# Performance work log

Measured on AMD Instinct MI355X. Metric: run time of the kernel, lower is better.

The kernel has to match this reference:

```python
import jax, jax.numpy as jnp
import numpy as np

B, Q, H = 1, 2048, 2048
NH, NKV, HD = 16, 8, 128
PAST = 2048
EPS = 1e-6


def rotate_half(x):
    x1, x2 = x[..., : x.shape[-1] // 2], x[..., x.shape[-1] // 2 :]
    return jnp.concatenate((-x2, x1), axis=-1)


def rms_norm(x, w, eps=EPS):
    var = jnp.mean(jnp.square(x.astype(jnp.float32)), axis=-1, keepdims=True)
    return (x * jax.lax.rsqrt(var + eps)) * w


def setup_inputs() -> dict:
    key = jax.random.key(0)
    ks = jax.random.split(key, 8)
    hidden_states = jax.random.normal(ks[0], (B, Q, H), jnp.float32)
    # RoPE tables for positions [PAST, PAST+Q)
    inv_freq = 1.0 / (1000000.0 ** (np.arange(0, HD, 2, dtype=np.float32) / HD))
    pos = np.arange(PAST, PAST + Q, dtype=np.float32)
    freqs = np.outer(pos, inv_freq)  # [Q, HD/2]
    emb = np.concatenate([freqs, freqs], axis=-1)  # [Q, HD]
    cos = jnp.asarray(np.cos(emb))[None].repeat(B, 0)
    sin = jnp.asarray(np.sin(emb))[None].repeat(B, 0)
    # causal additive mask over kv_len = PAST + Q
    q_idx = np.arange(Q)[:, None] + PAST
    kv_idx = np.arange(PAST + Q)[None, :]
    mask = np.where(kv_idx <= q_idx, 0.0, -1e9).astype(np.float32)
    attention_mask = jnp.asarray(mask)[None, None]  # [1,1,Q,PAST+Q]
    s = 1.0 / np.sqrt(H)
    return {
        "hidden_states": hidden_states,
        "cos": cos,
        "sin": sin,
        "attention_mask": attention_mask,
        "past_key": jax.random.normal(ks[1], (B, NKV, PAST, HD), jnp.float32),
        "past_value": jax.random.normal(ks[2], (B, NKV, PAST, HD), jnp.float32),
        "Wq": jax.random.normal(ks[3], (NH * HD, H), jnp.float32) * s,
        "Wk": jax.random.normal(ks[4], (NKV * HD, H), jnp.float32) * s,
        "Wv": jax.random.normal(ks[5], (NKV * HD, H), jnp.float32) * s,
        "Wo": jax.random.normal(ks[6], (NH * HD, NH * HD), jnp.float32) * s,
        "q_norm_w": jnp.ones((HD,), jnp.float32),
        "k_norm_w": jnp.ones((HD,), jnp.float32),
    }


def reference(hidden_states, cos, sin, attention_mask, past_key, past_value,
              Wq, Wk, Wv, Wo, q_norm_w, k_norm_w):
    bsz, q_len, _ = hidden_states.shape
    scaling = HD ** -0.5
    n_rep = NH // NKV

    q = jnp.einsum("bsh,dh->bsd", hidden_states, Wq).reshape(bsz, q_len, NH, HD).transpose(0, 2, 1, 3)
    k = jnp.einsum("bsh,dh->bsd", hidden_states, Wk).reshape(bsz, q_len, NKV, HD).transpose(0, 2, 1, 3)
    v = jnp.einsum("bsh,dh->bsd", hidden_states, Wv).reshape(bsz, q_len, NKV, HD).transpose(0, 2, 1, 3)

    q = rms_norm(q, q_norm_w)
    k = rms_norm(k, k_norm_w)

    c = cos[:, None]  # [B,1,Q,HD]
    s = sin[:, None]
    q = q * c + rotate_half(q) * s
    k = k * c + rotate_half(k) * s

    k_all = jnp.concatenate([past_key, k], axis=2)    # [B,NKV,PAST+Q,HD]
    v_all = jnp.concatenate([past_value, v], axis=2)
    new_key = k_all[:, :, -q_len:, :]
    new_value = v_all[:, :, -q_len:, :]

    kv_len = k_all.shape[2]
    k_rep = jnp.broadcast_to(k_all[:, :, None], (bsz, NKV, n_rep, kv_len, HD)).reshape(bsz, NH, kv_len, HD)
    v_rep = jnp.broadcast_to(v_all[:, :, None], (bsz, NKV, n_rep, kv_len, HD)).reshape(bsz, NH, kv_len, HD)

    scores = jnp.einsum("bhqd,bhkd->bhqk", q, k_rep) * scaling + attention_mask
    probs = jax.nn.softmax(scores.astype(jnp.float32), axis=-1).astype(q.dtype)
    out = jnp.einsum("bhqk,bhkd->bhqd", probs, v_rep)
    out = out.transpose(0, 2, 1, 3).reshape(bsz, q_len, NH * HD)
    out = jnp.einsum("bsd,hd->bsh", out, Wo)
    return out, new_key, new_value
```

## Files before the change

### kernel.cpp

```cpp
#include <hip/hip_runtime.h>
#include <hip/hip_bf16.h>

typedef __bf16 bf16_t;
typedef __bf16 bf16x8 __attribute__((ext_vector_type(8)));
typedef float f32x4 __attribute__((ext_vector_type(4)));

#define NH 16
#define NKV 8
#define HD 128
#define QLEN 2048
#define PASTLEN 2048
#define KVLEN 4096
#define NKOFF 4194304UL
#define NVOFF 6291456UL
#define SM_C1 0.12751741f
#define SM_C2 (-28.853900817779268f)

__device__ __forceinline__ void async16(const void* g, void* l) {
  __builtin_amdgcn_global_load_lds(
      (const __attribute__((address_space(1))) unsigned int*)g,
      (__attribute__((address_space(3))) unsigned int*)l, 16, 0, 0);
}

__device__ __forceinline__ bool detect_f32(const void* qw) {
  return *(const unsigned*)qw == 0x3F800000u;
}

__device__ __forceinline__ float ld1(const void* p, size_t i, bool f32) {
  return f32 ? ((const float*)p)[i] : (float)((const bf16_t*)p)[i];
}
__device__ __forceinline__ void st1(void* p, size_t i, bool f32, float v) {
  if (f32) ((float*)p)[i] = v; else ((bf16_t*)p)[i] = (bf16_t)v;
}
template <bool F32>
__device__ __forceinline__ uint4 ld8cvt(const void* p, size_t i) {
  if constexpr (!F32) {
    return *(const uint4*)((const bf16_t*)p + i);
  } else {
    const float* f = (const float*)p + i;
    float4 f0 = *(const float4*)f;
    float4 f1 = *(const float4*)(f + 4);
    union { bf16_t h[8]; uint4 u; } r;
    r.h[0] = (bf16_t)f0.x; r.h[1] = (bf16_t)f0.y; r.h[2] = (bf16_t)f0.z; r.h[3] = (bf16_t)f0.w;
    r.h[4] = (bf16_t)f1.x; r.h[5] = (bf16_t)f1.y; r.h[6] = (bf16_t)f1.z; r.h[7] = (bf16_t)f1.w;
    return r.u;
  }
}
__device__ __forceinline__ unsigned bfbits(float v) {
  bf16_t h = (bf16_t)v;
  union { bf16_t h; unsigned short u; } x; x.h = h;
  return (unsigned)x.u;
}

__global__ __launch_bounds__(256) void k_cvt4(
    const float* __restrict__ s0, const float* __restrict__ s1,
    const float* __restrict__ s2, const float* __restrict__ s3,
    bf16_t* __restrict__ d0, bf16_t* __restrict__ d1,
    bf16_t* __restrict__ d2, bf16_t* __restrict__ d3,
    const void* __restrict__ qw)
{
  if (!detect_f32(qw)) return;
  const int ten = blockIdx.y;
  const float* s; bf16_t* d; size_t n;
  switch (ten) {
    case 0:  s = s0; d = d0; n = 4194304; break;
    case 1:  s = s1; d = d1; n = 4194304; break;
    case 2:  s = s2; d = d2; n = 2097152; break;
    default: s = s3; d = d3; n = 2097152; break;
  }
  const size_t i = ((size_t)blockIdx.x * 256 + threadIdx.x) * 8;
  if (i >= n) return;
  uint4 v = ld8cvt<true>(s, i);
  *(uint4*)(d + i) = v;
}

template <int TM>
__device__ __forceinline__ void gemm_acc(
    const bf16_t* __restrict__ A, const bf16_t* __restrict__ B,
    int lda, int ldb, int m0, int n0, int K,
    bf16_t* __restrict__ As, bf16_t* __restrict__ Bs, f32x4 (*acc)[4])
{
  constexpr int MI   = TM / 32;
  constexpr int ACH  = TM / 32;
  constexpr int ABUF = TM * 64;

  const int tid  = threadIdx.x;
  const int lane = tid & 63;
  const int w    = tid >> 6;
  const int wm   = w >> 1, wn = w & 1;
  const int qid  = lane & 15, quad = lane >> 4;

  const int srow = tid >> 3, ssegp = tid & 7;

  auto stageA = [&](int kt, int buf) {
#pragma unroll
    for (int c = 0; c < ACH; c++) {
      const int row = c * 32 + srow;
      async16(A + (size_t)(m0 + row) * lda + kt * 64 + ((ssegp ^ (row & 7)) * 8),
              As + buf * ABUF + (size_t)(c * 256 + tid) * 8);
    }
  };
  auto stageB = [&](int kt, int buf) {
#pragma unroll
    for (int c = 0; c < 4; c++) {
      const int row = c * 32 + srow;
      async16(B + (size_t)(n0 + row) * ldb + kt * 64 + ((ssegp ^ (row & 7)) * 8),
              Bs + buf * 8192 + (size_t)(c * 256 + tid) * 8);
    }
  };

  stageA(0, 0); stageB(0, 0);
  const int NT = K >> 6;
  for (int kt = 0; kt < NT; kt++) {
    const int cur = kt & 1;
    if (kt + 1 < NT) {
      stageA(kt + 1, cur ^ 1);
      if constexpr (TM == 128) asm volatile("s_waitcnt vmcnt(4)" ::: "memory");
      else                     asm volatile("s_waitcnt vmcnt(2)" ::: "memory");
    } else {
      asm volatile("s_waitcnt vmcnt(0)" ::: "memory");
    }
    __builtin_amdgcn_s_barrier();

    {
      bf16x8 af[MI], bfr[4];
#pragma unroll
      for (int j = 0; j < 4; j++) {
        const int row = wn * 64 + j * 16 + qid;
        bfr[j] = *(const bf16x8*)(Bs + cur * 8192 + (size_t)row * 64 + ((quad ^ (row & 7)) * 8));
      }
#pragma unroll
      for (int i = 0; i < MI; i++) {
        const int row = wm * (TM / 2) + i * 16 + qid;
        af[i] = *(const bf16x8*)(As + cur * ABUF + (size_t)row * 64 + ((quad ^ (row & 7)) * 8));
      }
      __builtin_amdgcn_s_setprio(1);
#pragma unroll
      for (int i = 0; i < MI; i++)
#pragma unroll
        for (int j = 0; j < 4; j++)
          acc[i][j] = __builtin_amdgcn_mfma_f32_16x16x32_bf16(af[i], bfr[j], acc[i][j], 0, 0, 0);
      __builtin_amdgcn_s_setprio(0);
    }
    if (kt + 1 < NT) stageB(kt + 1, cur ^ 1);
    __builtin_amdgcn_s_barrier();

    {
      bf16x8 af[MI], bfr[4];
#pragma unroll
      for (int j = 0; j < 4; j++) {
        const int row = wn * 64 + j * 16 + qid;
        bfr[j] = *(const bf16x8*)(Bs + cur * 8192 + (size_t)row * 64 + (((4 + quad) ^ (row & 7)) * 8));
      }
#pragma unroll
      for (int i = 0; i < MI; i++) {
        const int row = wm * (TM / 2) + i * 16 + qid;
        af[i] = *(const bf16x8*)(As + cur * ABUF + (size_t)row * 64 + (((4 + quad) ^ (row & 7)) * 8));
      }
      __builtin_amdgcn_s_setprio(1);
#pragma unroll
      for (int i = 0; i < MI; i++)
#pragma unroll
        for (int j = 0; j < 4; j++)
          acc[i][j] = __builtin_amdgcn_mfma_f32_16x16x32_bf16(af[i], bfr[j], acc[i][j], 0, 0, 0);
      __builtin_amdgcn_s_setprio(0);
    }
    __builtin_amdgcn_s_barrier();
  }
}

__global__ __launch_bounds__(256) void k_gemm_qkv(
    const void* __restrict__ hs, const void* __restrict__ Wq,
    const void* __restrict__ Wk, const void* __restrict__ Wv,
    const bf16_t* __restrict__ hsb, const bf16_t* __restrict__ Wqb,
    const bf16_t* __restrict__ Wkb, const bf16_t* __restrict__ Wvb,
    const void* __restrict__ cs, const void* __restrict__ sn,
    const void* __restrict__ qw, const void* __restrict__ kw,
    bf16_t* __restrict__ qb, bf16_t* __restrict__ kc, void* __restrict__ dout)
{
  __shared__ __align__(16) char smem[67072];
  bf16_t* As = (bf16_t*)smem;
  bf16_t* Bs = (bf16_t*)(smem + 32768);
  float (*xs)[129]   = (float(*)[129])smem;
  float (*rsum)[128] = (float(*)[128])(smem + 66048);

  const bool f = detect_f32(qw);
  const bf16_t* A = f ? hsb : (const bf16_t*)hs;
  const int bx = blockIdx.x, by = blockIdx.y;
  const bf16_t* B; int n0;
  if (bx < 16)      { B = f ? Wqb : (const bf16_t*)Wq; n0 = bx * 128; }
  else if (bx < 24) { B = f ? Wkb : (const bf16_t*)Wk; n0 = (bx - 16) * 128; }
  else              { B = f ? Wvb : (const bf16_t*)Wv; n0 = (bx - 24) * 128; }

  f32x4 acc[4][4] = {};
  gemm_acc<128>(A, B, 2048, 2048, by * 128, n0, 2048, As, Bs, acc);

  const int tid = threadIdx.x, lane = tid & 63, w = tid >> 6;
  const int wm = w >> 1, wn = w & 1, qid = lane & 15, quad = lane >> 4;

  if (bx >= 24) {
    const int h = bx - 24;
#pragma unroll
    for (int i = 0; i < 4; i++)
#pragma unroll
      for (int j = 0; j < 4; j++) {
        const int rl = wm * 64 + i * 16 + quad * 4;
        const int d  = wn * 64 + j * 16 + qid;
#pragma unroll
        for (int r = 0; r < 4; r++) {
          const int s = by * 128 + rl + r;
          st1(dout, NVOFF + ((size_t)h * QLEN + s) * HD + d, f, acc[i][j][r]);
        }
      }
    return;
  }

  float rs[4][4];
#pragma unroll
  for (int i = 0; i < 4; i++)
#pragma unroll
    for (int r = 0; r < 4; r++) {
      float v = 0.f;
#pragma unroll
      for (int j = 0; j < 4; j++) v += acc[i][j][r] * acc[i][j][r];
#pragma unroll
      for (int o = 1; o < 16; o <<= 1) v += __shfl_xor(v, o, 64);
      rs[i][r] = v;
    }
#pragma unroll
  for (int i = 0; i < 4; i++)
#pragma unroll
    for (int j = 0; j < 4; j++) {
      const int rl = wm * 64 + i * 16 + quad * 4;
      const int d  = wn * 64 + j * 16 + qid;
#pragma unroll
      for (int r = 0; r < 4; r++) xs[rl + r][d] = acc[i][j][r];
    }
  if (qid == 0) {
#pragma unroll
    for (int i = 0; i < 4; i++)
#pragma unroll
      for (int r = 0; r < 4; r++)
        rsum[wn][wm * 64 + i * 16 + quad * 4 + r] = rs[i][r];
  }
  __syncthreads();
  const void* wgt = (bx < 16) ? qw : kw;
#pragma unroll
  for (int i = 0; i < 4; i++)
#pragma unroll
    for (int r = 0; r < 4; r++) {
      const int rl = wm * 64 + i * 16 + quad * 4 + r;
      const int s  = by * 128 + rl;
      const float inv = rsqrtf((rsum[0][rl] + rsum[1][rl]) * (1.0f / 128.0f) + 1e-6f);
#pragma unroll
      for (int j = 0; j < 4; j++) {
        const int d = wn * 64 + j * 16 + qid;
        const float x  = acc[i][j][r];
        const float xp = xs[rl][d ^ 64];
        const float y  = x  * inv * ld1(wgt, d, f);
        const float yp = xp * inv * ld1(wgt, d ^ 64, f);
        const float cv = ld1(cs, (size_t)s * HD + d, f);
        const float sv = ld1(sn, (size_t)s * HD + d, f);
        const float o  = (d < 64) ? y * cv - yp * sv : y * cv + yp * sv;
        if (bx < 16) {
          qb[(size_t)s * 2048 + bx * HD + d] = (bf16_t)o;
        } else {
          const int hk = bx - 16;
          st1(dout, NKOFF + ((size_t)hk * QLEN + s) * HD + d, f, o);
          kc[((size_t)hk * KVLEN + PASTLEN + s) * HD + d] = (bf16_t)o;
        }
      }
    }
}

__global__ __launch_bounds__(256) void k_gemm_o(
    const bf16_t* __restrict__ aout, const void* __restrict__ Wo,
    const bf16_t* __restrict__ Wob, void* __restrict__ dout,
    const void* __restrict__ qw)
{
  __shared__ __align__(16) char smem[49152];
  bf16_t* As = (bf16_t*)smem;
  bf16_t* Bs = (bf16_t*)(smem + 16384);
  const bool f = detect_f32(qw);
  const bf16_t* B = f ? Wob : (const bf16_t*)Wo;
  f32x4 acc[2][4] = {};
  gemm_acc<64>(aout, B, 2048, 2048, blockIdx.y * 64, blockIdx.x * 128, 2048, As, Bs, acc);

  const int tid = threadIdx.x, lane = tid & 63, w = tid >> 6;
  const int wm = w >> 1, wn = w & 1, qid = lane & 15, quad = lane >> 4;
#pragma unroll
  for (int i = 0; i < 2; i++)
#pragma unroll
    for (int j = 0; j < 4; j++) {
      const int rr = blockIdx.y * 64 + wm * 32 + i * 16 + quad * 4;
      const int cc = blockIdx.x * 128 + wn * 64 + j * 16 + qid;
#pragma unroll
      for (int r = 0; r < 4; r++)
        st1(dout, (size_t)(rr + r) * 2048 + cc, f, acc[i][j][r]);
    }
}

template <bool F>
__device__ __forceinline__ void prep_body(
    const void* __restrict__ pk, const void* __restrict__ pv,
    const void* __restrict__ dout,
    bf16_t* __restrict__ kc, bf16_t* __restrict__ vt,
    unsigned (*tile)[65])
{
  const int tid = threadIdx.x;
  const int hk = blockIdx.x >> 5, kvt = blockIdx.x & 31;
  const int kv0 = kvt * 128;

  if (kv0 < PASTLEN) {
    const size_t base = ((size_t)hk * PASTLEN + kv0) * HD;
    bf16_t* dst = kc + ((size_t)hk * KVLEN + kv0) * HD;
#pragma unroll
    for (int p = 0; p < 8; p++) {
      const int id = p * 256 + tid;
      const int r = id >> 4, c8 = (id & 15) * 8;
      uint4 vv = ld8cvt<F>(pk, base + (size_t)r * HD + c8);
      *(uint4*)(dst + (size_t)r * HD + c8) = vv;
    }
  }

  const void* src; size_t base;
  if (kv0 < PASTLEN) { src = pv;   base = ((size_t)hk * PASTLEN + kv0) * HD; }
  else               { src = dout; base = NVOFF + ((size_t)hk * QLEN + (kv0 - PASTLEN)) * HD; }
#pragma unroll
  for (int p = 0; p < 4; p++) {
    const int id = p * 256 + tid;
    const int r = id >> 4, e8 = (id & 15) * 8;
    if constexpr (!F) {
      uint4 a = *(const uint4*)((const bf16_t*)src + base + (size_t)(2 * r) * HD + e8);
      uint4 b = *(const uint4*)((const bf16_t*)src + base + (size_t)(2 * r + 1) * HD + e8);
      unsigned av[4] = {a.x, a.y, a.z, a.w}, bv[4] = {b.x, b.y, b.z, b.w};
#pragma unroll
      for (int q = 0; q < 4; q++) {
        tile[e8 + 2 * q][r]     = (av[q] & 0xffffu) | (bv[q] << 16);
        tile[e8 + 2 * q + 1][r] = (av[q] >> 16)     | (bv[q] & 0xffff0000u);
      }
    } else {
      const float* fa = (const float*)src + base + (size_t)(2 * r) * HD + e8;
      const float* fb = (const float*)src + base + (size_t)(2 * r + 1) * HD + e8;
#pragma unroll
      for (int e = 0; e < 8; e++)
        tile[e8 + e][r] = bfbits(fa[e]) | (bfbits(fb[e]) << 16);
    }
  }
  __syncthreads();
#pragma unroll
  for (int p = 0; p < 8; p++) {
    const int id = p * 256 + tid;
    const int e = id >> 4, c4 = (id & 15) * 4;
    uint4 wv;
    if (c4 & 8) {
      wv.x = tile[e][c4 + 2]; wv.y = tile[e][c4 + 3]; wv.z = tile[e][c4];     wv.w = tile[e][c4 + 1];
    } else {
      wv.x = tile[e][c4];     wv.y = tile[e][c4 + 1]; wv.z = tile[e][c4 + 2]; wv.w = tile[e][c4 + 3];
    }
    *(uint4*)(vt + ((size_t)hk * HD + e) * KVLEN + kv0 + c4 * 2) = wv;
  }
}
__global__ __launch_bounds__(256) void k_prep_kv(
    const void* __restrict__ pk, const void* __restrict__ pv,
    const void* __restrict__ dout,
    bf16_t* __restrict__ kc, bf16_t* __restrict__ vt,
    const float* __restrict__ Wo, bf16_t* __restrict__ Wob,
    const void* __restrict__ qw)
{
  __shared__ unsigned tile[128][65];
  const int bx = blockIdx.x;
  if (bx >= 256) {
    if (!detect_f32(qw)) return;
    const size_t i = ((size_t)(bx - 256) * 256 + threadIdx.x) * 8;
    uint4 v = ld8cvt<true>(Wo, i);
    *(uint4*)(Wob + i) = v;
    return;
  }
  if (detect_f32(qw)) prep_body<true>(pk, pv, dout, kc, vt, tile);
  else                prep_body<false>(pk, pv, dout, kc, vt, tile);
}

__global__ __launch_bounds__(256, 2) void k_attn(
    const bf16_t* __restrict__ qb, const bf16_t* __restrict__ kc,
    const bf16_t* __restrict__ vt, bf16_t* __restrict__ aout)
{
  __shared__ bf16_t ks[2][64 * 128];
  __shared__ bf16_t vs[2][128 * 64];
  __shared__ float  lsx[2][64];

  const int tid = threadIdx.x, lane = tid & 63, w = tid >> 6;
  const int qid = lane & 15, quad = lane >> 4;
  const int qg = w & 1;
  const int kh = w >> 1;
  const int bx = blockIdx.x;
  const int h  = ((bx & 7) << 1) | (bx >> 3);
  const int hk = h >> 1;
  const int by = blockIdx.y;
  const int qt = (by < 16) ? by : 47 - by;
  const int q0 = qt * 64;

  bf16x8 qf[2][4];
#pragma unroll
  for (int i = 0; i < 2; i++)
#pragma unroll
    for (int kst = 0; kst < 4; kst++)
      qf[i][kst] = *(const bf16x8*)(qb + (size_t)(q0 + qg * 32 + i * 16 + qid) * 2048
                                       + h * HD + kst * 32 + quad * 8);

  f32x4 Oacc[2][8] = {};
  float lsum[2] = {0.f, 0.f};

  const int J = quad >> 1;
  int bpa[4];
#pragma unroll
  for (int s = 0; s < 4; s++)
    bpa[s] = 4 * (qid + 16 * ((2 * quad + ((s >> 1) ^ J)) & 3));

  const bf16_t* kbase = kc + (size_t)hk * KVLEN * HD;
  const bf16_t* vbase = vt + (size_t)hk * HD * KVLEN;
  const int r16 = tid >> 4, ksg = tid & 15;
  const int r8  = tid >> 3, vsg = tid & 7;
  const int nt = qt + 33;

  auto stage = [&](int t, int buf) {
    const int kv0 = t * 64;
#pragma unroll
    for (int c = 0; c < 4; c++) {
      const int kr = c * 16 + r16;
      async16(kbase + (size_t)(kv0 + kr) * HD + ((ksg ^ (kr & 7)) * 8),
              &ks[buf][(size_t)(c * 256 + tid) * 8]);
    }
#pragma unroll
    for (int c = 0; c < 4; c++) {
      const int vr = c * 32 + r8;
      async16(vbase + (size_t)vr * KVLEN + kv0 + ((vsg ^ (vr & 7)) * 8),
              &vs[buf][(size_t)(c * 256 + tid) * 8]);
    }
  };

  stage(0, 0);

  for (int t = 0; t < nt; ++t) {
    const int cur = t & 1;
    if (t + 1 < nt) {
      stage(t + 1, cur ^ 1);
      asm volatile("s_waitcnt vmcnt(8)" ::: "memory");
    } else {
      asm volatile("s_waitcnt vmcnt(0)" ::: "memory");
    }
    __builtin_amdgcn_s_barrier();

    const bf16_t* ksb = ks[cur];
    const bf16_t* vsb = vs[cur];
    const int kv0 = t * 64;

    f32x4 sf[2][2] = {};
    __builtin_amdgcn_s_setprio(1);
#pragma unroll
    for (int kst = 0; kst < 4; kst++) {
      bf16x8 kf[2];
#pragma unroll
      for (int j = 0; j < 2; j++)
        kf[j] = *(const bf16x8*)(ksb + (size_t)((kh * 2 + j) * 16 + qid) * 128
                                     + (((kst * 4 + quad) * 8) ^ ((qid & 7) * 8)));
#pragma unroll
      for (int i = 0; i < 2; i++)
#pragma unroll
        for (int j = 0; j < 2; j++)
          sf[i][j] = __builtin_amdgcn_mfma_f32_16x16x32_bf16(kf[j], qf[i][kst], sf[i][j], 0, 0, 0);
    }
    __builtin_amdgcn_s_setprio(0);

    const bool lastt = (t == nt - 1);
    bf16x8 pf[2];
#pragma unroll
    for (int i = 0; i < 2; i++) {
      const int qglob = q0 + qg * 32 + i * 16 + qid + PASTLEN;
      float pr[2][4];
#pragma unroll
      for (int j = 0; j < 2; j++) {
        const int kvb = kv0 + kh * 32 + j * 16 + quad * 4;
#pragma unroll
        for (int r = 0; r < 4; r++) {
          float v = fmaf(sf[i][j][r], SM_C1, SM_C2);
          if (lastt && (kvb + r) > qglob) v = -1e9f;
          const float p = exp2f(v);
          lsum[i] += p;
          pr[j][r] = p;
        }
      }
      unsigned pk00, pk01, pk10, pk11;
      asm("v_cvt_pk_bf16_f32 %0, %1, %2" : "=v"(pk00) : "v"(pr[0][0]), "v"(pr[0][1]));
      asm("v_cvt_pk_bf16_f32 %0, %1, %2" : "=v"(pk01) : "v"(pr[0][2]), "v"(pr[0][3]));
      asm("v_cvt_pk_bf16_f32 %0, %1, %2" : "=v"(pk10) : "v"(pr[1][0]), "v"(pr[1][1]));
      asm("v_cvt_pk_bf16_f32 %0, %1, %2" : "=v"(pk11) : "v"(pr[1][2]), "v"(pr[1][3]));
      const bool qodd = (quad & 1) != 0;
      const unsigned reg0 = qodd ? pk10 : pk00;
      const unsigned reg1 = qodd ? pk11 : pk01;
      const unsigned reg2 = qodd ? pk00 : pk10;
      const unsigned reg3 = qodd ? pk01 : pk11;
      union { unsigned u[4]; bf16x8 v; } pu;
      pu.u[0] = (unsigned)__builtin_amdgcn_ds_bpermute(bpa[0], (int)reg0);
      pu.u[1] = (unsigned)__builtin_amdgcn_ds_bpermute(bpa[1], (int)reg1);
      pu.u[2] = (unsigned)__builtin_amdgcn_ds_bpermute(bpa[2], (int)reg2);
      pu.u[3] = (unsigned)__builtin_amdgcn_ds_bpermute(bpa[3], (int)reg3);
      pf[i] = pu.v;
    }

    __builtin_amdgcn_s_setprio(1);
#pragma unroll
    for (int n = 0; n < 8; n++) {
      bf16x8 vf = *(const bf16x8*)(vsb + (size_t)(n * 16 + qid) * 64
                                       + (((kh * 4 + quad) * 8) ^ ((qid & 7) * 8)));
      Oacc[0][n] = __builtin_amdgcn_mfma_f32_16x16x32_bf16(pf[0], vf, Oacc[0][n], 0, 0, 0);
      Oacc[1][n] = __builtin_amdgcn_mfma_f32_16x16x32_bf16(pf[1], vf, Oacc[1][n], 0, 0, 0);
    }
    __builtin_amdgcn_s_setprio(0);
    __builtin_amdgcn_s_barrier();
  }

#pragma unroll
  for (int i = 0; i < 2; i++) {
    lsum[i] += __shfl_xor(lsum[i], 16, 64);
    lsum[i] += __shfl_xor(lsum[i], 32, 64);
  }
  if (quad == 0) {
    lsx[kh][qg * 32 + qid]      = lsum[0];
    lsx[kh][qg * 32 + 16 + qid] = lsum[1];
  }
  float* Osc = (float*)ks;
  if (kh == 1) {
#pragma unroll
    for (int i = 0; i < 2; i++)
#pragma unroll
      for (int n = 0; n < 8; n++)
#pragma unroll
        for (int r = 0; r < 4; r++)
          Osc[(size_t)qg * 4096 + (i * 16 + quad * 4 + r) * 128 + n * 16 + qid] = Oacc[i][n][r];
  }
  __syncthreads();
  if (kh == 0) {
#pragma unroll
    for (int i = 0; i < 2; i++) {
      float invl[4];
#pragma unroll
      for (int r = 0; r < 4; r++) {
        const int qq = qg * 32 + i * 16 + quad * 4 + r;
        invl[r] = 1.0f / (lsx[0][qq] + lsx[1][qq]);
      }
#pragma unroll
      for (int n = 0; n < 8; n++)
#pragma unroll
        for (int r = 0; r < 4; r++) {
          const float ot = Oacc[i][n][r]
            + Osc[(size_t)qg * 4096 + (i * 16 + quad * 4 + r) * 128 + n * 16 + qid];
          const int row = q0 + qg * 32 + i * 16 + quad * 4 + r;
          aout[(size_t)row * 2048 + h * HD + n * 16 + qid] = (bf16_t)(ot * invl[r]);
        }
    }
  }
}

extern "C" void kernel_launch(void* const* d_in, const int* in_sizes, int n_in,
                              void* d_out, int out_size, void* d_ws, size_t ws_size,
                              hipStream_t stream) {
  const void* hs = d_in[0];
  const void* cs = d_in[1];
  const void* sn = d_in[2];
  const void* pk = d_in[4];
  const void* pv = d_in[5];
  const void* Wq = d_in[6];
  const void* Wk = d_in[7];
  const void* Wv = d_in[8];
  const void* Wo = d_in[9];
  const void* qw = d_in[10];
  const void* kw = d_in[11];

  char* ws = (char*)d_ws;
  bf16_t* qb   = (bf16_t*)(ws);
  bf16_t* kc   = (bf16_t*)(ws + (size_t)8  * 1024 * 1024);
  bf16_t* hsb  = (bf16_t*)(ws + (size_t)16 * 1024 * 1024);
  bf16_t* vt   = (bf16_t*)(ws + (size_t)16 * 1024 * 1024);
  bf16_t* Wqb  = (bf16_t*)(ws + (size_t)24 * 1024 * 1024);
  bf16_t* aout = (bf16_t*)(ws + (size_t)24 * 1024 * 1024);
  bf16_t* Wkb  = (bf16_t*)(ws + (size_t)32 * 1024 * 1024);
  bf16_t* Wvb  = (bf16_t*)(ws + (size_t)36 * 1024 * 1024);
  bf16_t* Wob  = (bf16_t*)(ws + (size_t)32 * 1024 * 1024);

  hipLaunchKernelGGL(k_cvt4, dim3(2048, 4), dim3(256), 0, stream,
                     (const float*)hs, (const float*)Wq, (const float*)Wk, (const float*)Wv,
                     hsb, Wqb, Wkb, Wvb, qw);
  hipLaunchKernelGGL(k_gemm_qkv, dim3(32, 16), dim3(256), 0, stream,
                     hs, Wq, Wk, Wv, hsb, Wqb, Wkb, Wvb, cs, sn, qw, kw, qb, kc, d_out);
  hipLaunchKernelGGL(k_prep_kv, dim3(2304), dim3(256), 0, stream,
                     pk, pv, d_out, kc, vt, (const float*)Wo, Wob, qw);
  hipLaunchKernelGGL(k_attn, dim3(16, 32), dim3(256), 0, stream, qb, kc, vt, aout);
  hipLaunchKernelGGL(k_gemm_o, dim3(16, 32), dim3(256), 0, stream, aout, Wo, Wob, d_out, qw);
}
```

Baseline: 349.4 us.

## Rewrite QKV GEMM with 256x128 tiles, 512 threads, interleaved async prefetch

The fused QKV projection kernel now uses 512-thread blocks, each computing a 256x128 output tile, which halves the grid in M. Global-to-LDS async loads for the next K tile are split into chunks interleaved between the MFMA phases, so memory traffic overlaps compute. The RMSNorm/RoPE epilogue now stages the partner values as bf16 in a transposed LDS layout instead of fp32, which shrinks shared memory but loses precision on the rotated partner. The larger tile and LDS footprint (96KB) cut per-CU occupancy and leave fewer blocks (256) to fill the machine.

```diff
diff --git a/kernel.cpp b/kernel.cpp
--- a/kernel.cpp
+++ b/kernel.cpp
@@ -74,6 +74,209 @@
   *(uint4*)(d + i) = v;
 }
 
+__global__ __launch_bounds__(512) void k_gemm_qkv(
+    const void* __restrict__ hs, const void* __restrict__ Wq,
+    const void* __restrict__ Wk, const void* __restrict__ Wv,
+    const bf16_t* __restrict__ hsb, const bf16_t* __restrict__ Wqb,
+    const bf16_t* __restrict__ Wkb, const bf16_t* __restrict__ Wvb,
+    const void* __restrict__ cs, const void* __restrict__ sn,
+    const void* __restrict__ qw, const void* __restrict__ kw,
+    bf16_t* __restrict__ qb, bf16_t* __restrict__ kc, void* __restrict__ dout)
+{
+  __shared__ __align__(16) char smem[98304];
+  bf16_t* As = (bf16_t*)smem;
+  bf16_t* Bs = (bf16_t*)(smem + 65536);
+  bf16_t* xsb  = (bf16_t*)smem;
+  float*  rsum = (float*)(smem + 67584);
+
+  const bool f = detect_f32(qw);
+  const bf16_t* A = f ? hsb : (const bf16_t*)hs;
+  const int bx = blockIdx.x, by = blockIdx.y;
+  const bf16_t* B; int n0;
+  if (bx < 16)      { B = f ? Wqb : (const bf16_t*)Wq; n0 = bx * 128; }
+  else if (bx < 24) { B = f ? Wkb : (const bf16_t*)Wk; n0 = (bx - 16) * 128; }
+  else              { B = f ? Wvb : (const bf16_t*)Wv; n0 = (bx - 24) * 128; }
+  const int m0 = by * 256;
+
+  const int tid = threadIdx.x, lane = tid & 63, w = tid >> 6;
+  const int wm = w >> 1, wn = w & 1;
+  const int qid = lane & 15, quad = lane >> 4;
+  const int srow = tid >> 3, ssegp = tid & 7;
+
+  f32x4 acc[4][4] = {};
+
+  auto stA = [&](int kt, int c) {
+    const int row = c * 64 + srow;
+    async16(A + (size_t)(m0 + row) * 2048 + kt * 64 + ((ssegp ^ (row & 7)) * 8),
+            As + (kt & 1) * 16384 + (size_t)(c * 512 + tid) * 8);
+  };
+  auto stB = [&](int kt, int c) {
+    const int row = c * 64 + srow;
+    async16(B + (size_t)(n0 + row) * 2048 + kt * 64 + ((ssegp ^ (row & 7)) * 8),
+            Bs + (kt & 1) * 8192 + (size_t)(c * 512 + tid) * 8);
+  };
+
+  stA(0, 0); stA(0, 1); stA(0, 2); stA(0, 3); stB(0, 0); stB(0, 1);
+
+  const int NT = 32;
+  for (int kt = 0; kt < NT; kt++) {
+    const bf16_t* Ab = As + (kt & 1) * 16384;
+    const bf16_t* Bb = Bs + (kt & 1) * 8192;
+    bf16x8 af[4], bf2[2];
+
+    if (kt + 1 < NT) {
+      stA(kt + 1, 0); stA(kt + 1, 1);
+      asm volatile("s_waitcnt vmcnt(2)" ::: "memory");
+    } else {
+      asm volatile("s_waitcnt vmcnt(0)" ::: "memory");
+    }
+    __builtin_amdgcn_s_barrier();
+#pragma unroll
+    for (int i = 0; i < 4; i++) {
+      const int row = wm * 64 + i * 16 + qid;
+      af[i] = *(const bf16x8*)(Ab + (size_t)row * 64 + ((quad ^ (row & 7)) * 8));
+    }
+#pragma unroll
+    for (int j = 0; j < 2; j++) {
+      const int row = wn * 64 + j * 16 + qid;
+      bf2[j] = *(const bf16x8*)(Bb + (size_t)row * 64 + ((quad ^ (row & 7)) * 8));
+    }
+    __builtin_amdgcn_s_setprio(1);
+#pragma unroll
+    for (int i = 0; i < 4; i++)
+#pragma unroll
+      for (int j = 0; j < 2; j++)
+        acc[i][j] = __builtin_amdgcn_mfma_f32_16x16x32_bf16(af[i], bf2[j], acc[i][j], 0, 0, 0);
+    __builtin_amdgcn_s_setprio(0);
+    __builtin_amdgcn_s_barrier();
+
+    if (kt + 1 < NT) { stA(kt + 1, 2); stA(kt + 1, 3); }
+#pragma unroll
+    for (int j = 0; j < 2; j++) {
+      const int row = wn * 64 + (j + 2) * 16 + qid;
+      bf2[j] = *(const bf16x8*)(Bb + (size_t)row * 64 + ((quad ^ (row & 7)) * 8));
+    }
+    __builtin_amdgcn_s_setprio(1);
+#pragma unroll
+    for (int i = 0; i < 4; i++)
+#pragma unroll
+      for (int j = 0; j < 2; j++)
+        acc[i][j + 2] = __builtin_amdgcn_mfma_f32_16x16x32_bf16(af[i], bf2[j], acc[i][j + 2], 0, 0, 0);
+    __builtin_amdgcn_s_setprio(0);
+    __builtin_amdgcn_s_barrier();
+
+    if (kt + 1 < NT) { stB(kt + 1, 0); stB(kt + 1, 1); }
+#pragma unroll
+    for (int i = 0; i < 4; i++) {
+      const int row = wm * 64 + i * 16 + qid;
+      af[i] = *(const bf16x8*)(Ab + (size_t)row * 64 + (((4 + quad) ^ (row & 7)) * 8));
+    }
+#pragma unroll
+    for (int j = 0; j < 2; j++) {
+      const int row = wn * 64 + j * 16 + qid;
+      bf2[j] = *(const bf16x8*)(Bb + (size_t)row * 64 + (((4 + quad) ^ (row & 7)) * 8));
+    }
+    __builtin_amdgcn_s_setprio(1);
+#pragma unroll
+    for (int i = 0; i < 4; i++)
+#pragma unroll
+      for (int j = 0; j < 2; j++)
+        acc[i][j] = __builtin_amdgcn_mfma_f32_16x16x32_bf16(af[i], bf2[j], acc[i][j], 0, 0, 0);
+    __builtin_amdgcn_s_setprio(0);
+    __builtin_amdgcn_s_barrier();
+
+#pragma unroll
+    for (int j = 0; j < 2; j++) {
+      const int row = wn * 64 + (j + 2) * 16 + qid;
+      bf2[j] = *(const bf16x8*)(Bb + (size_t)row * 64 + (((4 + quad) ^ (row & 7)) * 8));
+    }
+    __builtin_amdgcn_s_setprio(1);
+#pragma unroll
+    for (int i = 0; i < 4; i++)
+#pragma unroll
+      for (int j = 0; j < 2; j++)
+        acc[i][j + 2] = __builtin_amdgcn_mfma_f32_16x16x32_bf16(af[i], bf2[j], acc[i][j + 2], 0, 0, 0);
+    __builtin_amdgcn_s_setprio(0);
+    __builtin_amdgcn_s_barrier();
+  }
+
+  if (bx >= 24) {
+    const int h = bx - 24;
+#pragma unroll
+    for (int i = 0; i < 4; i++)
+#pragma unroll
+      for (int j = 0; j < 4; j++) {
+        const int rl = wm * 64 + i * 16 + quad * 4;
+        const int d  = wn * 64 + j * 16 + qid;
+#pragma unroll
+        for (int r = 0; r < 4; r++) {
+          const int s = by * 256 + rl + r;
+          st1(dout, NVOFF + ((size_t)h * QLEN + s) * HD + d, f, acc[i][j][r]);
+        }
+      }
+    return;
+  }
+
+#pragma unroll
+  for (int i = 0; i < 4; i++)
+#pragma unroll
+    for (int r = 0; r < 4; r++) {
+      float v = 0.f;
+#pragma unroll
+      for (int j = 0; j < 4; j++) v += acc[i][j][r] * acc[i][j][r];
+#pragma unroll
+      for (int o = 1; o < 16; o <<= 1) v += __shfl_xor(v, o, 64);
+      if (qid == 0) rsum[wn * 256 + wm * 64 + i * 16 + quad * 4 + r] = v;
+    }
+#pragma unroll
+  for (int i = 0; i < 4; i++) {
+    const int rlb = wm * 64 + i * 16 + quad * 4;
+#pragma unroll
+    for (int j = 0; j < 4; j++) {
+      const int d = wn * 64 + j * 16 + qid;
+      union { bf16_t h[4]; unsigned long long u; } px;
+#pragma unroll
+      for (int r = 0; r < 4; r++) px.h[r] = (bf16_t)acc[i][j][r];
+      *(unsigned long long*)(xsb + (size_t)d * 264 + rlb) = px.u;
+    }
+  }
+  __syncthreads();
+  const void* wgt = (bx < 16) ? qw : kw;
+#pragma unroll
+  for (int i = 0; i < 4; i++) {
+    const int rlb = wm * 64 + i * 16 + quad * 4;
+    float inv[4];
+#pragma unroll
+    for (int r = 0; r < 4; r++)
+      inv[r] = rsqrtf((rsum[rlb + r] + rsum[256 + rlb + r]) * (1.0f / 128.0f) + 1e-6f);
+#pragma unroll
+    for (int j = 0; j < 4; j++) {
+      const int d = wn * 64 + j * 16 + qid;
+      const float wv  = ld1(wgt, d, f);
+      const float wvp = ld1(wgt, d ^ 64, f);
+      union { bf16_t h[4]; unsigned long long u; } xp;
+      xp.u = *(const unsigned long long*)(xsb + (size_t)(d ^ 64) * 264 + rlb);
+#pragma unroll
+      for (int r = 0; r < 4; r++) {
+        const int s = by * 256 + rlb + r;
+        const float x  = acc[i][j][r];
+        const float y  = x * inv[r] * wv;
+        const float yp = (float)xp.h[r] * inv[r] * wvp;
+        const float cv = ld1(cs, (size_t)s * HD + d, f);
+        const float sv = ld1(sn, (size_t)s * HD + d, f);
+        const float o  = (d < 64) ? y * cv - yp * sv : y * cv + yp * sv;
+        if (bx < 16) {
+          qb[(size_t)s * 2048 + bx * HD + d] = (bf16_t)o;
+        } else {
+          const int hk = bx - 16;
+          st1(dout, NKOFF + ((size_t)hk * QLEN + s) * HD + d, f, o);
+          kc[((size_t)hk * KVLEN + PASTLEN + s) * HD + d] = (bf16_t)o;
+        }
+      }
+    }
+  }
+}
+
 template <int TM>
 __device__ __forceinline__ void gemm_acc(
     const bf16_t* __restrict__ A, const bf16_t* __restrict__ B,
@@ -167,110 +370,6 @@
     }
     __builtin_amdgcn_s_barrier();
   }
-}
-
-__global__ __launch_bounds__(256) void k_gemm_qkv(
-    const void* __restrict__ hs, const void* __restrict__ Wq,
-    const void* __restrict__ Wk, const void* __restrict__ Wv,
-    const bf16_t* __restrict__ hsb, const bf16_t* __restrict__ Wqb,
-    const bf16_t* __restrict__ Wkb, const bf16_t* __restrict__ Wvb,
-    const void* __restrict__ cs, const void* __restrict__ sn,
-    const void* __restrict__ qw, const void* __restrict__ kw,
-    bf16_t* __restrict__ qb, bf16_t* __restrict__ kc, void* __restrict__ dout)
-{
-  __shared__ __align__(16) char smem[67072];
-  bf16_t* As = (bf16_t*)smem;
-  bf16_t* Bs = (bf16_t*)(smem + 32768);
-  float (*xs)[129]   = (float(*)[129])smem;
-  float (*rsum)[128] = (float(*)[128])(smem + 66048);
-
-  const bool f = detect_f32(qw);
-  const bf16_t* A = f ? hsb : (const bf16_t*)hs;
-  const int bx = blockIdx.x, by = blockIdx.y;
-  const bf16_t* B; int n0;
-  if (bx < 16)      { B = f ? Wqb : (const bf16_t*)Wq; n0 = bx * 128; }
-  else if (bx < 24) { B = f ? Wkb : (const bf16_t*)Wk; n0 = (bx - 16) * 128; }
-  else              { B = f ? Wvb : (const bf16_t*)Wv; n0 = (bx - 24) * 128; }
-
-  f32x4 acc[4][4] = {};
-  gemm_acc<128>(A, B, 2048, 2048, by * 128, n0, 2048, As, Bs, acc);
-
-  const int tid = threadIdx.x, lane = tid & 63, w = tid >> 6;
-  const int wm = w >> 1, wn = w & 1, qid = lane & 15, quad = lane >> 4;
-
-  if (bx >= 24) {
-    const int h = bx - 24;
-#pragma unroll
-    for (int i = 0; i < 4; i++)
-#pragma unroll
-      for (int j = 0; j < 4; j++) {
-        const int rl = wm * 64 + i * 16 + quad * 4;
-        const int d  = wn * 64 + j * 16 + qid;
-#pragma unroll
-        for (int r = 0; r < 4; r++) {
-          const int s = by * 128 + rl + r;
-          st1(dout, NVOFF + ((size_t)h * QLEN + s) * HD + d, f, acc[i][j][r]);
-        }
-      }
-    return;
-  }
-
-  float rs[4][4];
-#pragma unroll
-  for (int i = 0; i < 4; i++)
-#pragma unroll
-    for (int r = 0; r < 4; r++) {
-      float v = 0.f;
-#pragma unroll
-      for (int j = 0; j < 4; j++) v += acc[i][j][r] * acc[i][j][r];
-#pragma unroll
-      for (int o = 1; o < 16; o <<= 1) v += __shfl_xor(v, o, 64);
-      rs[i][r] = v;
-    }
-#pragma unroll
-  for (int i = 0; i < 4; i++)
-#pragma unroll
-    for (int j = 0; j < 4; j++) {
-      const int rl = wm * 64 + i * 16 + quad * 4;
-      const int d  = wn * 64 + j * 16 + qid;
-#pragma unroll
-      for (int r = 0; r < 4; r++) xs[rl + r][d] = acc[i][j][r];
-    }
-  if (qid == 0) {
-#pragma unroll
-    for (int i = 0; i < 4; i++)
-#pragma unroll
-      for (int r = 0; r < 4; r++)
-        rsum[wn][wm * 64 + i * 16 + quad * 4 + r] = rs[i][r];
-  }
-  __syncthreads();
-  const void* wgt = (bx < 16) ? qw : kw;
-#pragma unroll
-  for (int i = 0; i < 4; i++)
-#pragma unroll
-    for (int r = 0; r < 4; r++) {
-      const int rl = wm * 64 + i * 16 + quad * 4 + r;
-      const int s  = by * 128 + rl;
-      const float inv = rsqrtf((rsum[0][rl] + rsum[1][rl]) * (1.0f / 128.0f) + 1e-6f);
-#pragma unroll
-      for (int j = 0; j < 4; j++) {
-        const int d = wn * 64 + j * 16 + qid;
-        const float x  = acc[i][j][r];
-        const float xp = xs[rl][d ^ 64];
-        const float y  = x  * inv * ld1(wgt, d, f);
-        const float yp = xp * inv * ld1(wgt, d ^ 64, f);
-        const float cv = ld1(cs, (size_t)s * HD + d, f);
-        const float sv = ld1(sn, (size_t)s * HD + d, f);
-        const float o  = (d < 64) ? y * cv - yp * sv : y * cv + yp * sv;
-        if (bx < 16) {
-          qb[(size_t)s * 2048 + bx * HD + d] = (bf16_t)o;
-        } else {
-          const int hk = bx - 16;
-          st1(dout, NKOFF + ((size_t)hk * QLEN + s) * HD + d, f, o);
-          kc[((size_t)hk * KVLEN + PASTLEN + s) * HD + d] = (bf16_t)o;
-        }
-      }
-    }
 }
 
 __global__ __launch_bounds__(256) void k_gemm_o(
@@ -591,7 +690,7 @@
   hipLaunchKernelGGL(k_cvt4, dim3(2048, 4), dim3(256), 0, stream,
                      (const float*)hs, (const float*)Wq, (const float*)Wk, (const float*)Wv,
                      hsb, Wqb, Wkb, Wvb, qw);
-  hipLaunchKernelGGL(k_gemm_qkv, dim3(32, 16), dim3(256), 0, stream,
+  hipLaunchKernelGGL(k_gemm_qkv, dim3(32, 8), dim3(512), 0, stream,
                      hs, Wq, Wk, Wv, hsb, Wqb, Wkb, Wvb, cs, sn, qw, kw, qb, kc, d_out);
   hipLaunchKernelGGL(k_prep_kv, dim3(2304), dim3(256), 0, stream,
                      pk, pv, d_out, kc, vt, (const float*)Wo, Wob, qw);
```

Result: no change. 346.5 us (-0.8%).
